# Kernel tuning notes

Hardware: AMD Instinct MI355X
Metric: run time of the kernel (lower is better)

Reference implementation:

```python
import jax, jax.numpy as jnp
import numpy as np

B, LQ, LK, D, H, DK, DV = 4, 2048, 2048, 1024, 16, 64, 64
TEMP = float(np.sqrt(DK))
LN_EPS = 1e-5


def setup_inputs() -> dict:
    key = jax.random.key(0)
    ks = jax.random.split(key, 12)
    std_qk = float(np.sqrt(2.0 / (D + DK)))
    std_v = float(np.sqrt(2.0 / (D + DV)))
    std_fc = float(np.sqrt(2.0 / (H * DV + D)))  # xavier normal
    return {
        "q": jax.random.normal(ks[0], (B, LQ, D), jnp.float32),
        "k": jax.random.normal(ks[1], (B, LK, D), jnp.float32),
        "v": jax.random.normal(ks[2], (B, LK, D), jnp.float32),
        "key_padding_mask": jax.random.randint(ks[3], (B, LK), 0, 2) > 0,
        "Wq": jax.random.normal(ks[4], (D, H * DK), jnp.float32) * std_qk,
        "bq": jnp.zeros((H * DK,), jnp.float32),
        "Wk": jax.random.normal(ks[5], (D, H * DK), jnp.float32) * std_qk,
        "bk": jnp.zeros((H * DK,), jnp.float32),
        "Wv": jax.random.normal(ks[6], (D, H * DV), jnp.float32) * std_v,
        "bv": jnp.zeros((H * DV,), jnp.float32),
        "Wo": jax.random.normal(ks[7], (H * DV, D), jnp.float32) * std_fc,
        "bo": jnp.zeros((D,), jnp.float32),
        "ln_g": jnp.ones((D,), jnp.float32),
        "ln_b": jnp.zeros((D,), jnp.float32),
    }


def reference(q, k, v, key_padding_mask, Wq, bq, Wk, bk, Wv, bv, Wo, bo, ln_g, ln_b):
    residual = q
    # projections -> [B, H, L, dh]
    qh = (q @ Wq + bq).reshape(B, LQ, H, DK).transpose(0, 2, 1, 3)
    kh = (k @ Wk + bk).reshape(B, LK, H, DK).transpose(0, 2, 1, 3)
    vh = (v @ Wv + bv).reshape(B, LK, H, DV).transpose(0, 2, 1, 3)
    # scaled dot-product attention, mask padded keys with -inf pre-softmax
    logits = jnp.einsum("bhqd,bhkd->bhqk", qh, kh) / TEMP
    logits = jnp.where(key_padding_mask[:, None, None, :], -jnp.inf, logits)
    attn = jax.nn.softmax(logits, axis=-1)  # masked entries -> 0
    out = jnp.einsum("bhqk,bhkd->bhqd", attn, vh)
    # concat heads (head-major per original permute) -> [B, LQ, H*DV]
    out = out.transpose(0, 2, 1, 3).reshape(B, LQ, H * DV)
    out = out @ Wo + bo
    out = out + residual  # skip connection (d_out == d_model)
    # LayerNorm over last dim
    mu = out.mean(-1, keepdims=True)
    var = ((out - mu) ** 2).mean(-1, keepdims=True)
    out = (out - mu) * jax.lax.rsqrt(var + LN_EPS) * ln_g + ln_b
    attn_avg = attn.mean(axis=1)  # average over heads -> [B, LQ, LK]
    return out, attn_avg
```

## Files before the change

### kernel.cpp

```cpp
#include <hip/hip_runtime.h>
#include <hip/hip_bf16.h>
#include <math.h>

#define B_    4
#define LQ_   2048
#define LK_   2048
#define D_    1024
#define H_    16
#define LN_EPS_ 1e-5f
#define NEGINF (-__builtin_inff())
#define QSCALE 0.18033688011112042f

typedef __attribute__((ext_vector_type(8))) short bf16x8;
typedef __attribute__((ext_vector_type(4))) short bf16x4;
typedef __attribute__((ext_vector_type(4))) float f32x4;

#define MFMA(a, b, c) __builtin_amdgcn_mfma_f32_16x16x32_bf16(a, b, c, 0, 0, 0)

#if __has_builtin(__builtin_amdgcn_exp2f)
#define EXP2(x) __builtin_amdgcn_exp2f(x)
#else
#define EXP2(x) __expf((x) * 0.6931471805599453f)
#endif

__device__ __forceinline__ short f2bf(float f) {
    union { __hip_bfloat16 h; short s; } u;
    u.h = __float2bfloat16(f);
    return u.s;
}

__device__ __forceinline__ void gld16(const short* g, short* l) {
    __builtin_amdgcn_global_load_lds(
        (const __attribute__((address_space(1))) void*)g,
        (__attribute__((address_space(3))) void*)l, 16, 0, 0);
}

__device__ __forceinline__ void xcd_swz(int gx, int* bx, int* by) {
    const int lin = *bx + gx * (*by);
    const int n8  = (gx * 512 / gx) >> 3;
    const int nl  = (lin & 7) * n8 + (lin >> 3);
    *bx = nl % gx;
    *by = nl / gx;
}

__global__ __launch_bounds__(256) void scan_kernel(
    const int* __restrict__ mask, int* __restrict__ idx, int* __restrict__ pos,
    int* __restrict__ cnt, float* __restrict__ maskc)
{
    const int b = blockIdx.x;
    const int t = threadIdx.x;
    const int lane = t & 63, wid = t >> 6;
    __shared__ int wsum[4];
    const int base = b * 2048 + t * 8;

    int fl[8]; int loc = 0;
    #pragma unroll
    for (int j = 0; j < 8; ++j) { fl[j] = (mask[base + j] == 0) ? 1 : 0; loc += fl[j]; }

    int inc = loc;
    #pragma unroll
    for (int d = 1; d < 64; d <<= 1) {
        const int n = __shfl_up(inc, d);
        if (lane >= d) inc += n;
    }
    if (lane == 63) wsum[wid] = inc;
    __syncthreads();
    int wbase = 0;
    for (int i = 0; i < wid; ++i) wbase += wsum[i];
    const int total = wsum[0] + wsum[1] + wsum[2] + wsum[3];

    int e = wbase + inc - loc;
    #pragma unroll
    for (int j = 0; j < 8; ++j) {
        const int p = t * 8 + j;
        if (fl[j]) { idx[b * 2048 + e] = p; pos[base + j] = e; ++e; }
        else        pos[base + j] = -1;
        maskc[base + j] = (p < total) ? 0.f : NEGINF;
        if (p >= total) idx[base + j] = 0;
    }
    if (t == 0) cnt[b] = total;
}

__global__ __launch_bounds__(256) void cast_x_kernel(
    const float* __restrict__ q, const float* __restrict__ k, const float* __restrict__ v,
    const int* __restrict__ mask,
    short* __restrict__ Xq, short* __restrict__ Xk, short* __restrict__ Xv,
    float* __restrict__ maskf)
{
    const int which = blockIdx.y;
    const float* src = which == 0 ? q : (which == 1 ? k : v);
    short* dst       = which == 0 ? Xq : (which == 1 ? Xk : Xv);
    const int t = threadIdx.x;
    const size_t i = ((size_t)blockIdx.x * 256 + t) * 8;
    const float4 a = *reinterpret_cast<const float4*>(src + i);
    const float4 c = *reinterpret_cast<const float4*>(src + i + 4);
    bf16x8 o;
    o[0] = f2bf(a.x); o[1] = f2bf(a.y); o[2] = f2bf(a.z); o[3] = f2bf(a.w);
    o[4] = f2bf(c.x); o[5] = f2bf(c.y); o[6] = f2bf(c.z); o[7] = f2bf(c.w);
    *reinterpret_cast<bf16x8*>(dst + i) = o;
    if (which == 0) {
        const int gid = blockIdx.x * 256 + t;
        if (gid < B_ * LK_) maskf[gid] = (mask[gid] != 0) ? NEGINF : 0.0f;
    }
}

__global__ __launch_bounds__(256) void cast_wt_kernel(
    const float* __restrict__ Wq, const float* __restrict__ Wk,
    const float* __restrict__ Wv, const float* __restrict__ Wo,
    short* __restrict__ Wtq, short* __restrict__ Wtk,
    short* __restrict__ Wtv, short* __restrict__ Wto)
{
    const int which = blockIdx.z;
    const float* W = which == 0 ? Wq : (which == 1 ? Wk : (which == 2 ? Wv : Wo));
    short* Wt      = which == 0 ? Wtq : (which == 1 ? Wtk : (which == 2 ? Wtv : Wto));

    __shared__ float T[64][65];
    const int t = threadIdx.x;
    const int k0 = blockIdx.x * 64, n0 = blockIdx.y * 64;
    {
        const int row = t >> 2, cq = (t & 3) * 16;
        #pragma unroll
        for (int i = 0; i < 4; ++i) {
            const float4 v4 = *reinterpret_cast<const float4*>(&W[(size_t)(k0 + row) * 1024 + n0 + cq + i * 4]);
            T[row][cq + i * 4 + 0] = v4.x; T[row][cq + i * 4 + 1] = v4.y;
            T[row][cq + i * 4 + 2] = v4.z; T[row][cq + i * 4 + 3] = v4.w;
        }
    }
    __syncthreads();
    const int nl = t >> 2, kq = (t & 3) * 16;
    bf16x8 o0, o1;
    #pragma unroll
    for (int j = 0; j < 8; ++j) {
        o0[j] = f2bf(T[kq + j][nl]);
        o1[j] = f2bf(T[kq + 8 + j][nl]);
    }
    *reinterpret_cast<bf16x8*>(&Wt[(size_t)(n0 + nl) * 1024 + k0 + kq]) = o0;
    *reinterpret_cast<bf16x8*>(&Wt[(size_t)(n0 + nl) * 1024 + k0 + kq + 8]) = o1;
}

__global__ __launch_bounds__(256) void proj_kernel(
    const short* __restrict__ Xq, const short* __restrict__ Xk, const short* __restrict__ Xv,
    const short* __restrict__ Wtq, const short* __restrict__ Wtk, const short* __restrict__ Wtv,
    const float* __restrict__ bq, const float* __restrict__ bk, const float* __restrict__ bv,
    const int* __restrict__ pos,
    short* __restrict__ qh, short* __restrict__ kh, short* __restrict__ vTc)
{
    const int which = blockIdx.z;
    const short* A  = which == 0 ? Xq : (which == 1 ? Xk : Xv);
    const short* Bt = which == 0 ? Wtq : (which == 1 ? Wtk : Wtv);
    const float* bias = which == 0 ? bq : (which == 1 ? bk : bv);

    __shared__ short Al[4096];
    __shared__ short Bl[4096];

    const int t = threadIdx.x;
    const int lane = t & 63, w = t >> 6;
    const int wm = w >> 1, wn = w & 1;
    const int g = lane >> 4, r16 = lane & 15;

    int bx = blockIdx.x, by = blockIdx.y;
    xcd_swz(8, &bx, &by);
    const int m0 = by * 128, n0 = bx * 128;

    f32x4 acc[4][4] = {};

    for (int k0 = 0; k0 < 1024; k0 += 32) {
        __syncthreads();
        #pragma unroll
        for (int i = 0; i < 2; ++i) {
            const int row = i * 64 + (t >> 2);
            const int cl = (t & 3) ^ ((row >> 1) & 3);
            gld16(A  + (size_t)(m0 + row) * 1024 + k0 + cl * 8, Al + i * 2048 + t * 8);
            gld16(Bt + (size_t)(n0 + row) * 1024 + k0 + cl * 8, Bl + i * 2048 + t * 8);
        }
        __syncthreads();

        bf16x8 af[4], bf[4];
        #pragma unroll
        for (int mf = 0; mf < 4; ++mf) {
            const int row = wm * 64 + mf * 16 + r16;
            af[mf] = *reinterpret_cast<const bf16x8*>(
                (const char*)Al + row * 64 + (((g ^ ((row >> 1) & 3))) << 4));
        }
        #pragma unroll
        for (int nf = 0; nf < 4; ++nf) {
            const int row = wn * 64 + nf * 16 + r16;
            bf[nf] = *reinterpret_cast<const bf16x8*>(
                (const char*)Bl + row * 64 + (((g ^ ((row >> 1) & 3))) << 4));
        }
        #pragma unroll
        for (int mf = 0; mf < 4; ++mf)
            #pragma unroll
            for (int nf = 0; nf < 4; ++nf)
                acc[mf][nf] = MFMA(af[mf], bf[nf], acc[mf][nf]);
    }

    if (which < 2) {
        #pragma unroll
        for (int nf = 0; nf < 4; ++nf) {
            const int n = n0 + wn * 64 + nf * 16 + r16;
            const int h = n >> 6, dh = n & 63;
            const float bn = bias[n];
            #pragma unroll
            for (int mf = 0; mf < 4; ++mf) {
                #pragma unroll
                for (int r = 0; r < 4; ++r) {
                    const int m = m0 + wm * 64 + mf * 16 + 4 * g + r;
                    const int bb = m >> 11, l = m & 2047;
                    float vf = acc[mf][nf][r] + bn;
                    if (which == 0) vf *= QSCALE;
                    ((which == 0) ? qh : kh)[(((size_t)(bb * H_ + h)) * LQ_ + l) * 64 + dh] = f2bf(vf);
                }
            }
        }
    } else {
        int posr[4][4], bbr[4][4];
        #pragma unroll
        for (int mf = 0; mf < 4; ++mf)
            #pragma unroll
            for (int r = 0; r < 4; ++r) {
                const int m = m0 + wm * 64 + mf * 16 + 4 * g + r;
                const int bb = m >> 11, l = m & 2047;
                bbr[mf][r] = bb;
                posr[mf][r] = pos[bb * 2048 + l];
            }
        #pragma unroll
        for (int nf = 0; nf < 4; ++nf) {
            const int n = n0 + wn * 64 + nf * 16 + r16;
            const int h = n >> 6, dh = n & 63;
            const float bn = bias[n];
            #pragma unroll
            for (int mf = 0; mf < 4; ++mf) {
                #pragma unroll
                for (int r = 0; r < 4; ++r) {
                    const int pc = posr[mf][r];
                    if (pc >= 0)
                        vTc[(((size_t)(bbr[mf][r] * H_ + h)) * 64 + dh) * (size_t)LK_ + pc] =
                            f2bf(acc[mf][nf][r] + bn);
                }
            }
        }
    }
}

__global__ __launch_bounds__(256) void flash_kernel(
    const short* __restrict__ qh, const short* __restrict__ kh, const short* __restrict__ vTc,
    const int* __restrict__ idx, const int* __restrict__ cnt, const float* __restrict__ maskc,
    short* __restrict__ ctx, float* __restrict__ mOut, float* __restrict__ sOut)
{
    int bx = blockIdx.x, by = blockIdx.y;
    xcd_swz(32, &bx, &by);
    const int q0 = bx * 64;
    const int h  = by;
    const int b  = blockIdx.z;

    __shared__ short Kl[2][4096];
    __shared__ short Vl[2][4096];

    const int t = threadIdx.x;
    const int lane = t & 63, w = t >> 6;
    const int g = lane >> 4, q16 = lane & 15;

    const short* kbase = kh + (size_t)(b * H_ + h) * LK_ * 64;
    const short* vbase = vTc + (size_t)(b * H_ + h) * 64 * (size_t)LK_;
    const int*   idxb  = idx + b * 2048;
    const int nt = (cnt[b] + 63) >> 6;

    bf16x8 qf0, qf1;
    {
        const short* qrow = qh + ((size_t)(b * H_ + h) * LQ_ + q0 + w * 16 + q16) * 64;
        qf0 = *reinterpret_cast<const bf16x8*>(qrow + 8 * g);
        qf1 = *reinterpret_cast<const bf16x8*>(qrow + 32 + 8 * g);
    }

    f32x4 mlast[4] = {};
    if (nt > 0) {
        #pragma unroll
        for (int kb = 0; kb < 4; ++kb)
            mlast[kb] = *reinterpret_cast<const f32x4*>(
                maskc + b * 2048 + (nt - 1) * 64 + kb * 16 + 4 * g);
    }

    const int srw = t >> 3, scl = t & 7;

    f32x4 ot[4] = {};
    float m_run = NEGINF, l_run = 0.f;

    if (nt > 0) {
        #pragma unroll
        for (int i = 0; i < 2; ++i) {
            const int row = i * 32 + srw;
            const int cl = scl ^ (row & 7);
            const int orig = idxb[row];
            gld16(kbase + (size_t)orig * 64 + cl * 8, Kl[0] + i * 2048 + t * 8);
            gld16(vbase + (size_t)row * LK_ + cl * 8, Vl[0] + i * 2048 + t * 8);
        }
    }
    __syncthreads();

    int cur = 0;
    for (int kt = 0; kt < nt; ++kt) {
        if (kt + 1 < nt) {
            const int kn = (kt + 1) * 64;
            #pragma unroll
            for (int i = 0; i < 2; ++i) {
                const int row = i * 32 + srw;
                const int cl = scl ^ (row & 7);
                const int orig = idxb[kn + row];
                gld16(kbase + (size_t)orig * 64 + cl * 8, Kl[cur ^ 1] + i * 2048 + t * 8);
                gld16(vbase + (size_t)row * LK_ + kn + cl * 8, Vl[cur ^ 1] + i * 2048 + t * 8);
            }
        }
        const bool lastt = (kt == nt - 1);

        float lg[4][4];
        const short* klp = Kl[cur];
        __builtin_amdgcn_s_setprio(1);
        #pragma unroll
        for (int kb = 0; kb < 4; ++kb) {
            const int krow = kb * 16 + q16;
            const char* rowp = (const char*)klp + krow * 128;
            const int sw = (krow & 7) << 4;
            const bf16x8 kf0 = *reinterpret_cast<const bf16x8*>(rowp + ((g << 4) ^ sw));
            const bf16x8 kf1 = *reinterpret_cast<const bf16x8*>(rowp + (((4 + g) << 4) ^ sw));
            f32x4 s = lastt ? mlast[kb] : (f32x4){0.f, 0.f, 0.f, 0.f};
            s = MFMA(kf0, qf0, s);
            s = MFMA(kf1, qf1, s);
            #pragma unroll
            for (int r = 0; r < 4; ++r) lg[kb][r] = s[r];
        }
        __builtin_amdgcn_s_setprio(0);

        float tm = NEGINF;
        #pragma unroll
        for (int kb = 0; kb < 4; ++kb)
            #pragma unroll
            for (int r = 0; r < 4; ++r) tm = fmaxf(tm, lg[kb][r]);
        tm = fmaxf(tm, __shfl_xor(tm, 16));
        tm = fmaxf(tm, __shfl_xor(tm, 32));

        const bool skip = __all(tm <= m_run + 8.0f);
        if (!skip) {
            const float m_new = fmaxf(m_run, tm);
            const float alpha = (m_run == NEGINF) ? 0.f : EXP2(m_run - m_new);
            #pragma unroll
            for (int fc = 0; fc < 4; ++fc)
                #pragma unroll
                for (int r = 0; r < 4; ++r) ot[fc][r] *= alpha;
            l_run *= alpha;
            m_run = m_new;
        }
        const float m_use = (m_run == NEGINF) ? 0.f : m_run;

        float p[4][4];
        float ls = 0.f;
        #pragma unroll
        for (int kb = 0; kb < 4; ++kb)
            #pragma unroll
            for (int r = 0; r < 4; ++r) { p[kb][r] = EXP2(lg[kb][r] - m_use); ls += p[kb][r]; }
        ls += __shfl_xor(ls, 16);
        ls += __shfl_xor(ls, 32);
        l_run += ls;

        bf16x8 pb[2];
        #pragma unroll
        for (int r = 0; r < 4; ++r) {
            pb[0][r]     = f2bf(p[0][r]);
            pb[0][4 + r] = f2bf(p[1][r]);
            pb[1][r]     = f2bf(p[2][r]);
            pb[1][4 + r] = f2bf(p[3][r]);
        }

        const short* vlp = Vl[cur];
        __builtin_amdgcn_s_setprio(1);
        #pragma unroll
        for (int fc = 0; fc < 4; ++fc) {
            const int dvrow = fc * 16 + q16;
            const char* rowp = (const char*)vlp + dvrow * 128;
            const int sw = (dvrow & 7) << 4;
            #pragma unroll
            for (int tt = 0; tt < 2; ++tt) {
                const bf16x4 va = *reinterpret_cast<const bf16x4*>(rowp + ((64 * tt + 8 * g) ^ sw));
                const bf16x4 vb = *reinterpret_cast<const bf16x4*>(rowp + ((64 * tt + 32 + 8 * g) ^ sw));
                bf16x8 af;
                af[0] = va[0]; af[1] = va[1]; af[2] = va[2]; af[3] = va[3];
                af[4] = vb[0]; af[5] = vb[1]; af[6] = vb[2]; af[7] = vb[3];
                ot[fc] = MFMA(af, pb[tt], ot[fc]);
            }
        }
        __builtin_amdgcn_s_setprio(0);

        __syncthreads();
        cur ^= 1;
    }

    const float rs = (l_run > 0.f) ? 1.0f / l_run : 0.f;
    short* crow = ctx + ((size_t)b * LQ_ + q0 + w * 16 + q16) * (size_t)(H_ * 64) + h * 64;
    #pragma unroll
    for (int fc = 0; fc < 4; ++fc) {
        bf16x4 o4;
        #pragma unroll
        for (int r = 0; r < 4; ++r) o4[r] = f2bf(ot[fc][r] * rs);
        *reinterpret_cast<bf16x4*>(crow + fc * 16 + 4 * g) = o4;
    }
    if (lane < 16) {
        const size_t idxo = (size_t)(b * H_ + h) * LQ_ + q0 + w * 16 + lane;
        mOut[idxo] = m_run;
        sOut[idxo] = l_run;
    }
}

__global__ __launch_bounds__(512) void avg_kernel(
    const short* __restrict__ qh, const short* __restrict__ kh,
    const float* __restrict__ maskf,
    const float* __restrict__ mS, const float* __restrict__ sS,
    float* __restrict__ attn_avg)
{
    const int k0 = blockIdx.x * 64;
    const int q0 = blockIdx.y * 128;
    const int b  = blockIdx.z;

    __shared__ short Kl[2][4096];

    const int t = threadIdx.x;
    const int lane = t & 63, w = t >> 6;
    const int g = lane >> 4, q16 = lane & 15;

    f32x4 mk[4];
    #pragma unroll
    for (int kb = 0; kb < 4; ++kb)
        mk[kb] = *reinterpret_cast<const f32x4*>(maskf + b * LK_ + k0 + kb * 16 + 4 * g);

    const int srw = t >> 3, scl = t & 7;
    const int cl = scl ^ (srw & 7);
    const short* kbb = kh + ((size_t)b * H_ * LK_ + k0) * 64;

    const short* qbase = qh + ((size_t)b * H_ * LQ_ + q0 + w * 16 + q16) * 64;
    const size_t stbase = (size_t)b * H_ * LQ_ + q0 + w * 16 + q16;

    {
        gld16(kbb + (size_t)srw * 64 + cl * 8, Kl[0] + t * 8);
    }
    bf16x8 qc0 = *reinterpret_cast<const bf16x8*>(qbase + 8 * g);
    bf16x8 qc1 = *reinterpret_cast<const bf16x8*>(qbase + 32 + 8 * g);
    float mc = mS[stbase], sc = sS[stbase];
    __syncthreads();

    f32x4 acc[4] = {};
    int cur = 0;
    for (int hh = 0; hh < H_; ++hh) {
        bf16x8 qn0, qn1; float mn = 0.f, sn = 0.f;
        if (hh + 1 < H_) {
            gld16(kbb + (size_t)(hh + 1) * LK_ * 64 + (size_t)srw * 64 + cl * 8,
                  Kl[cur ^ 1] + t * 8);
            const short* qp = qbase + (size_t)(hh + 1) * LQ_ * 64;
            qn0 = *reinterpret_cast<const bf16x8*>(qp + 8 * g);
            qn1 = *reinterpret_cast<const bf16x8*>(qp + 32 + 8 * g);
            mn = mS[stbase + (size_t)(hh + 1) * LQ_];
            sn = sS[stbase + (size_t)(hh + 1) * LQ_];
        }

        const float madj = (mc == NEGINF || sc <= 0.f)
                               ? __builtin_inff() : mc + __log2f(sc);

        const short* klp = Kl[cur];
        __builtin_amdgcn_s_setprio(1);
        #pragma unroll
        for (int kb = 0; kb < 4; ++kb) {
            const int krow = kb * 16 + q16;
            const char* rowp = (const char*)klp + krow * 128;
            const int sw = (krow & 7) << 4;
            const bf16x8 kf0 = *reinterpret_cast<const bf16x8*>(rowp + ((g << 4) ^ sw));
            const bf16x8 kf1 = *reinterpret_cast<const bf16x8*>(rowp + (((4 + g) << 4) ^ sw));
            f32x4 s = mk[kb];
            s = MFMA(kf0, qc0, s);
            s = MFMA(kf1, qc1, s);
            #pragma unroll
            for (int r = 0; r < 4; ++r)
                acc[kb][r] += EXP2(s[r] - madj);
        }
        __builtin_amdgcn_s_setprio(0);

        __syncthreads();
        if (hh + 1 < H_) { qc0 = qn0; qc1 = qn1; mc = mn; sc = sn; }
        cur ^= 1;
    }

    const float scale = 1.0f / (float)H_;
    float* orow = attn_avg + ((size_t)b * LQ_ + q0 + w * 16 + q16) * (size_t)LK_ + k0;
    #pragma unroll
    for (int kb = 0; kb < 4; ++kb) {
        f32x4 o = acc[kb];
        o[0] *= scale; o[1] *= scale; o[2] *= scale; o[3] *= scale;
        *reinterpret_cast<f32x4*>(orow + kb * 16 + 4 * g) = o;
    }
}

__global__ __launch_bounds__(256) void outproj_kernel(
    const short* __restrict__ ctxIn, const short* __restrict__ Wto,
    const float* __restrict__ bo, const float* __restrict__ resid,
    float* __restrict__ preln)
{
    __shared__ short Al[4096];
    __shared__ short Bl[4096];

    const int t = threadIdx.x;
    const int lane = t & 63, w = t >> 6;
    const int wm = w >> 1, wn = w & 1;
    const int g = lane >> 4, r16 = lane & 15;

    int bx = blockIdx.x, by = blockIdx.y;
    xcd_swz(8, &bx, &by);
    const int m0 = by * 128, n0 = bx * 128;

    f32x4 acc[4][4] = {};

    for (int k0 = 0; k0 < 1024; k0 += 32) {
        __syncthreads();
        #pragma unroll
        for (int i = 0; i < 2; ++i) {
            const int row = i * 64 + (t >> 2);
            const int cl = (t & 3) ^ ((row >> 1) & 3);
            gld16(ctxIn + (size_t)(m0 + row) * 1024 + k0 + cl * 8, Al + i * 2048 + t * 8);
            gld16(Wto   + (size_t)(n0 + row) * 1024 + k0 + cl * 8, Bl + i * 2048 + t * 8);
        }
        __syncthreads();

        bf16x8 af[4], bf[4];
        #pragma unroll
        for (int mf = 0; mf < 4; ++mf) {
            const int row = wm * 64 + mf * 16 + r16;
            af[mf] = *reinterpret_cast<const bf16x8*>(
                (const char*)Al + row * 64 + (((g ^ ((row >> 1) & 3))) << 4));
        }
        #pragma unroll
        for (int nf = 0; nf < 4; ++nf) {
            const int row = wn * 64 + nf * 16 + r16;
            bf[nf] = *reinterpret_cast<const bf16x8*>(
                (const char*)Bl + row * 64 + (((g ^ ((row >> 1) & 3))) << 4));
        }
        #pragma unroll
        for (int mf = 0; mf < 4; ++mf)
            #pragma unroll
            for (int nf = 0; nf < 4; ++nf)
                acc[mf][nf] = MFMA(af[mf], bf[nf], acc[mf][nf]);
    }

    #pragma unroll
    for (int nf = 0; nf < 4; ++nf) {
        const int n = n0 + wn * 64 + nf * 16 + r16;
        const float bn = bo[n];
        #pragma unroll
        for (int mf = 0; mf < 4; ++mf) {
            #pragma unroll
            for (int r = 0; r < 4; ++r) {
                const size_t m = m0 + wm * 64 + mf * 16 + 4 * g + r;
                preln[m * 1024 + n] = acc[mf][nf][r] + bn + resid[m * 1024 + n];
            }
        }
    }
}

__global__ __launch_bounds__(256) void ln_kernel(
    const float* __restrict__ xin, const float* __restrict__ gam,
    const float* __restrict__ bet, float* __restrict__ out)
{
    const size_t row = blockIdx.x;
    const int t = threadIdx.x;
    const float4 v = *reinterpret_cast<const float4*>(&xin[row * 1024 + t * 4]);

    float s  = v.x + v.y + v.z + v.w;
    float ss = v.x * v.x + v.y * v.y + v.z * v.z + v.w * v.w;
    #pragma unroll
    for (int w = 1; w < 64; w <<= 1) { s += __shfl_xor(s, w); ss += __shfl_xor(ss, w); }

    __shared__ float rs_[4], rss_[4];
    if ((t & 63) == 0) { rs_[t >> 6] = s; rss_[t >> 6] = ss; }
    __syncthreads();
    s  = rs_[0] + rs_[1] + rs_[2] + rs_[3];
    ss = rss_[0] + rss_[1] + rss_[2] + rss_[3];

    const float mean = s * (1.0f / 1024.0f);
    const float var  = ss * (1.0f / 1024.0f) - mean * mean;
    const float rstd = rsqrtf(var + LN_EPS_);

    const float4 g4 = *reinterpret_cast<const float4*>(&gam[t * 4]);
    const float4 b4 = *reinterpret_cast<const float4*>(&bet[t * 4]);
    float4 o;
    o.x = (v.x - mean) * rstd * g4.x + b4.x;
    o.y = (v.y - mean) * rstd * g4.y + b4.y;
    o.z = (v.z - mean) * rstd * g4.z + b4.z;
    o.w = (v.w - mean) * rstd * g4.w + b4.w;
    *reinterpret_cast<float4*>(&out[row * 1024 + t * 4]) = o;
}

extern "C" void kernel_launch(void* const* d_in, const int* in_sizes, int n_in,
                              void* d_out, int out_size, void* d_ws, size_t ws_size,
                              hipStream_t stream)
{
    const float* q    = (const float*)d_in[0];
    const float* k    = (const float*)d_in[1];
    const float* v    = (const float*)d_in[2];
    const int*   mask = (const int*)d_in[3];
    const float* Wq   = (const float*)d_in[4];
    const float* bq   = (const float*)d_in[5];
    const float* Wk   = (const float*)d_in[6];
    const float* bk   = (const float*)d_in[7];
    const float* Wv   = (const float*)d_in[8];
    const float* bv   = (const float*)d_in[9];
    const float* Wo   = (const float*)d_in[10];
    const float* bo   = (const float*)d_in[11];
    const float* lng  = (const float*)d_in[12];
    const float* lnb  = (const float*)d_in[13];

    float* out      = (float*)d_out;
    float* attn_avg = out + (size_t)B_ * LQ_ * D_;

    const size_t XSZ = (size_t)B_ * LQ_ * D_;
    const size_t WSZ = (size_t)D_ * D_;

    short* Xq  = (short*)d_ws;
    short* Xk  = Xq + XSZ;
    short* Xv  = Xk + XSZ;
    short* Wtq = Xv + XSZ;
    short* Wtk = Wtq + WSZ;
    short* Wtv = Wtk + WSZ;
    short* Wto = Wtv + WSZ;
    short* qh  = Wto + WSZ;
    short* kh  = qh + XSZ;
    short* vTc = kh + XSZ;
    float* mSt = (float*)(vTc + XSZ);
    float* sSt = mSt + (size_t)B_ * H_ * LQ_;
    float* maskf = sSt + (size_t)B_ * H_ * LQ_;
    float* maskc = maskf + (size_t)B_ * LK_;
    int*   idx   = (int*)(maskc + (size_t)B_ * LK_);
    int*   pos   = idx + (size_t)B_ * LK_;
    int*   cnt   = pos + (size_t)B_ * LK_;
    float* preln = (float*)qh;
    short* ctx   = Xv;

    scan_kernel<<<dim3(B_), 256, 0, stream>>>(mask, idx, pos, cnt, maskc);
    cast_x_kernel<<<dim3(4096, 3), 256, 0, stream>>>(q, k, v, mask, Xq, Xk, Xv, maskf);
    cast_wt_kernel<<<dim3(16, 16, 4), 256, 0, stream>>>(Wq, Wk, Wv, Wo, Wtq, Wtk, Wtv, Wto);

    proj_kernel<<<dim3(8, 64, 3), 256, 0, stream>>>(Xq, Xk, Xv, Wtq, Wtk, Wtv,
                                                    bq, bk, bv, pos, qh, kh, vTc);

    flash_kernel<<<dim3(32, 16, 4), 256, 0, stream>>>(qh, kh, vTc, idx, cnt, maskc,
                                                      ctx, mSt, sSt);

    avg_kernel<<<dim3(32, 16, 4), 512, 0, stream>>>(qh, kh, maskf, mSt, sSt, attn_avg);

    outproj_kernel<<<dim3(8, 64), 256, 0, stream>>>(ctx, Wto, bo, q, preln);

    ln_kernel<<<8192, 256, 0, stream>>>(preln, lng, lnb, out);
}
```

Measured before the change: 310.3 us.

## Compact unmasked keys in head-averaged attention kernel and zero-fill masked columns

```diff
diff --git a/kernel.cpp b/kernel.cpp
--- a/kernel.cpp
+++ b/kernel.cpp
@@ -43,6 +43,12 @@
     *by = nl / gx;
 }
 
+__global__ __launch_bounds__(256) void zfill_kernel(float* __restrict__ p)
+{
+    const size_t i = ((size_t)blockIdx.x * 256 + threadIdx.x) * 4;
+    *reinterpret_cast<f32x4*>(p + i) = (f32x4){0.f, 0.f, 0.f, 0.f};
+}
+
 __global__ __launch_bounds__(256) void scan_kernel(
     const int* __restrict__ mask, int* __restrict__ idx, int* __restrict__ pos,
     int* __restrict__ cnt, float* __restrict__ maskc)
@@ -83,9 +89,7 @@
 
 __global__ __launch_bounds__(256) void cast_x_kernel(
     const float* __restrict__ q, const float* __restrict__ k, const float* __restrict__ v,
-    const int* __restrict__ mask,
-    short* __restrict__ Xq, short* __restrict__ Xk, short* __restrict__ Xv,
-    float* __restrict__ maskf)
+    short* __restrict__ Xq, short* __restrict__ Xk, short* __restrict__ Xv)
 {
     const int which = blockIdx.y;
     const float* src = which == 0 ? q : (which == 1 ? k : v);
@@ -98,10 +102,6 @@
     o[0] = f2bf(a.x); o[1] = f2bf(a.y); o[2] = f2bf(a.z); o[3] = f2bf(a.w);
     o[4] = f2bf(c.x); o[5] = f2bf(c.y); o[6] = f2bf(c.z); o[7] = f2bf(c.w);
     *reinterpret_cast<bf16x8*>(dst + i) = o;
-    if (which == 0) {
-        const int gid = blockIdx.x * 256 + t;
-        if (gid < B_ * LK_) maskf[gid] = (mask[gid] != 0) ? NEGINF : 0.0f;
-    }
 }
 
 __global__ __launch_bounds__(256) void cast_wt_kernel(
@@ -412,13 +412,19 @@
 
 __global__ __launch_bounds__(512) void avg_kernel(
     const short* __restrict__ qh, const short* __restrict__ kh,
-    const float* __restrict__ maskf,
+    const int* __restrict__ idx, const int* __restrict__ cnt,
+    const float* __restrict__ maskc,
     const float* __restrict__ mS, const float* __restrict__ sS,
     float* __restrict__ attn_avg)
 {
-    const int k0 = blockIdx.x * 64;
-    const int q0 = blockIdx.y * 128;
-    const int b  = blockIdx.z;
+    const int b = blockIdx.z;
+    const int cntb = cnt[b];
+    const int nt = (cntb + 63) >> 6;
+    if ((int)blockIdx.x >= nt) return;
+
+    const int kc0 = blockIdx.x * 64;
+    const int q0  = blockIdx.y * 128;
+    const bool lastt = ((int)blockIdx.x == nt - 1);
 
     __shared__ short Kl[2][4096];
 
@@ -429,17 +435,22 @@
     f32x4 mk[4];
     #pragma unroll
     for (int kb = 0; kb < 4; ++kb)
-        mk[kb] = *reinterpret_cast<const f32x4*>(maskf + b * LK_ + k0 + kb * 16 + 4 * g);
+        mk[kb] = lastt ? *reinterpret_cast<const f32x4*>(maskc + b * 2048 + kc0 + kb * 16 + 4 * g)
+                       : (f32x4){0.f, 0.f, 0.f, 0.f};
 
     const int srw = t >> 3, scl = t & 7;
     const int cl = scl ^ (srw & 7);
-    const short* kbb = kh + ((size_t)b * H_ * LK_ + k0) * 64;
+    const int* idxb = idx + b * 2048;
+    const int orig = idxb[kc0 + srw];
+    const short* kpb = kh + (size_t)b * H_ * (size_t)LK_ * 64
+                          + (size_t)orig * 64 + cl * 8;
+    const size_t hstep = (size_t)LK_ * 64;
 
     const short* qbase = qh + ((size_t)b * H_ * LQ_ + q0 + w * 16 + q16) * 64;
     const size_t stbase = (size_t)b * H_ * LQ_ + q0 + w * 16 + q16;
 
     {
-        gld16(kbb + (size_t)srw * 64 + cl * 8, Kl[0] + t * 8);
+        gld16(kpb, Kl[0] + t * 8);
     }
     bf16x8 qc0 = *reinterpret_cast<const bf16x8*>(qbase + 8 * g);
     bf16x8 qc1 = *reinterpret_cast<const bf16x8*>(qbase + 32 + 8 * g);
@@ -451,8 +462,7 @@
     for (int hh = 0; hh < H_; ++hh) {
         bf16x8 qn0, qn1; float mn = 0.f, sn = 0.f;
         if (hh + 1 < H_) {
-            gld16(kbb + (size_t)(hh + 1) * LK_ * 64 + (size_t)srw * 64 + cl * 8,
-                  Kl[cur ^ 1] + t * 8);
+            gld16(kpb + (size_t)(hh + 1) * hstep, Kl[cur ^ 1] + t * 8);
             const short* qp = qbase + (size_t)(hh + 1) * LQ_ * 64;
             qn0 = *reinterpret_cast<const bf16x8*>(qp + 8 * g);
             qn1 = *reinterpret_cast<const bf16x8*>(qp + 32 + 8 * g);
@@ -487,12 +497,14 @@
     }
 
     const float scale = 1.0f / (float)H_;
-    float* orow = attn_avg + ((size_t)b * LQ_ + q0 + w * 16 + q16) * (size_t)LK_ + k0;
+    float* orow = attn_avg + ((size_t)b * LQ_ + q0 + w * 16 + q16) * (size_t)LK_;
     #pragma unroll
     for (int kb = 0; kb < 4; ++kb) {
-        f32x4 o = acc[kb];
-        o[0] *= scale; o[1] *= scale; o[2] *= scale; o[3] *= scale;
-        *reinterpret_cast<f32x4*>(orow + kb * 16 + 4 * g) = o;
+        #pragma unroll
+        for (int r = 0; r < 4; ++r) {
+            const int kc = kc0 + kb * 16 + 4 * g + r;
+            if (kc < cntb) orow[idxb[kc]] = acc[kb][r] * scale;
+        }
     }
 }
 
@@ -631,16 +643,16 @@
     short* vTc = kh + XSZ;
     float* mSt = (float*)(vTc + XSZ);
     float* sSt = mSt + (size_t)B_ * H_ * LQ_;
-    float* maskf = sSt + (size_t)B_ * H_ * LQ_;
-    float* maskc = maskf + (size_t)B_ * LK_;
+    float* maskc = sSt + (size_t)B_ * H_ * LQ_;
     int*   idx   = (int*)(maskc + (size_t)B_ * LK_);
     int*   pos   = idx + (size_t)B_ * LK_;
     int*   cnt   = pos + (size_t)B_ * LK_;
     float* preln = (float*)qh;
     short* ctx   = Xv;
 
+    zfill_kernel<<<dim3((B_ * LQ_ * LK_) / (256 * 4)), 256, 0, stream>>>(attn_avg);
     scan_kernel<<<dim3(B_), 256, 0, stream>>>(mask, idx, pos, cnt, maskc);
-    cast_x_kernel<<<dim3(4096, 3), 256, 0, stream>>>(q, k, v, mask, Xq, Xk, Xv, maskf);
+    cast_x_kernel<<<dim3(4096, 3), 256, 0, stream>>>(q, k, v, Xq, Xk, Xv);
     cast_wt_kernel<<<dim3(16, 16, 4), 256, 0, stream>>>(Wq, Wk, Wv, Wo, Wtq, Wtk, Wtv, Wto);
 
     proj_kernel<<<dim3(8, 64, 3), 256, 0, stream>>>(Xq, Xk, Xv, Wtq, Wtk, Wtv,
@@ -649,7 +661,8 @@
     flash_kernel<<<dim3(32, 16, 4), 256, 0, stream>>>(qh, kh, vTc, idx, cnt, maskc,
                                                       ctx, mSt, sSt);
 
-    avg_kernel<<<dim3(32, 16, 4), 512, 0, stream>>>(qh, kh, maskf, mSt, sSt, attn_avg);
+    avg_kernel<<<dim3(32, 16, 4), 512, 0, stream>>>(qh, kh, idx, cnt, maskc,
+                                                    mSt, sSt, attn_avg);
 
     outproj_kernel<<<dim3(8, 64), 256, 0, stream>>>(ctx, Wto, bo, q, preln);
 
```

Result: slower. 358.6 us (+15.6%).
